# Optimization experiments

Hardware: AMD Instinct MI355X
Metric: run time of the kernel (lower is better)

## Reference

```python
import jax, jax.numpy as jnp
import numpy as np

D_MODEL = 1024
NUM_HEADS = 16
D_HEAD = D_MODEL // NUM_HEADS


def setup_inputs() -> dict:
    key = jax.random.key(0)
    ks = jax.random.split(key, 12)
    B, S, D = 2, 2048, D_MODEL
    s = 1.0 / np.sqrt(D)
    return {
        "Q": jax.random.normal(ks[0], (B, S, D), jnp.float32),
        "K": jax.random.normal(ks[1], (B, S, D), jnp.float32),
        "V": jax.random.normal(ks[2], (B, S, D), jnp.float32),
        "mask": jnp.ones((B, 1, 1, S), jnp.int32),
        "Wq": jax.random.normal(ks[3], (D, D), jnp.float32) * s,
        "bq": jnp.zeros((D,), jnp.float32),
        "Wk": jax.random.normal(ks[4], (D, D), jnp.float32) * s,
        "bk": jnp.zeros((D,), jnp.float32),
        "Wv": jax.random.normal(ks[5], (D, D), jnp.float32) * s,
        "bv": jnp.zeros((D,), jnp.float32),
        "Wo": jax.random.normal(ks[6], (D, D), jnp.float32) * s,
        "bo": jnp.zeros((D,), jnp.float32),
    }


def reference(Q, K, V, mask, Wq, bq, Wk, bk, Wv, bv, Wo, bo):
    B, Sq, D = Q.shape
    H, Dh = NUM_HEADS, D_HEAD
    # projections (torch Linear: x @ W.T + b), then split heads -> (B,H,S,Dh)
    q = (Q @ Wq.T + bq).reshape(B, Sq, H, Dh).transpose(0, 2, 1, 3)
    k = (K @ Wk.T + bk).reshape(B, -1, H, Dh).transpose(0, 2, 1, 3)
    v = (V @ Wv.T + bv).reshape(B, -1, H, Dh).transpose(0, 2, 1, 3)
    scores = jnp.einsum("bhqd,bhkd->bhqk", q, k) / jnp.sqrt(jnp.float32(Dh))
    scores = jnp.where(mask == 0, jnp.float32(-1e9), scores)
    attn = jax.nn.softmax(scores, axis=-1)
    out = jnp.einsum("bhqk,bhkd->bhqd", attn, v)  # (B,H,Sq,Dh)
    out = out.transpose(0, 2, 1, 3).reshape(B, Sq, D)
    out = out @ Wo.T + bo
    return out, attn
```

## Files before the change

### kernel.cpp

```cpp
#include <hip/hip_runtime.h>

#define BB 2
#define SS 2048
#define DD 1024
#define HH 16
#define DHH 64
#define NN (BB*SS)
#define NNDD ((size_t)NN * DD)
#define DDDD ((size_t)DD * DD)

typedef __attribute__((ext_vector_type(8))) __bf16 bf16x8;
typedef __attribute__((ext_vector_type(4))) float f32x4;
typedef union { unsigned int u[4]; bf16x8 v; } bfu8;

__device__ __forceinline__ unsigned short f2bf(float f) {
  unsigned int u = __float_as_uint(f);
  return (unsigned short)((u + 0x7FFFu + ((u >> 16) & 1u)) >> 16);
}
__device__ __forceinline__ float bf2f(unsigned short h) {
  return __uint_as_float(((unsigned int)h) << 16);
}

__device__ __forceinline__ void gl_lds16(const unsigned short* g, unsigned short* l) {
  __builtin_amdgcn_global_load_lds(
      (const __attribute__((address_space(1))) unsigned int*)g,
      (__attribute__((address_space(3))) unsigned int*)l, 16, 0, 0);
}

#define MFMA16(a, b, c) __builtin_amdgcn_mfma_f32_16x16x32_bf16((a), (b), (c), 0, 0, 0)

__global__ __launch_bounds__(256) void split3(
    const float* __restrict__ x0, const float* __restrict__ x1,
    const float* __restrict__ x2, unsigned short* __restrict__ outbase,
    size_t zstride, int n4) {
  const float* x = (blockIdx.z == 0) ? x0 : (blockIdx.z == 1 ? x1 : x2);
  unsigned short* hi = outbase + (size_t)blockIdx.z * zstride;
  unsigned short* lo = hi + (size_t)n4 * 4;
  int i = blockIdx.x * 256 + threadIdx.x;
  int stride = gridDim.x * 256;
  for (; i < n4; i += stride) {
    float4 v = ((const float4*)x)[i];
    float f[4] = {v.x, v.y, v.z, v.w};
    unsigned short hs[4], ls[4];
#pragma unroll
    for (int j = 0; j < 4; ++j) {
      hs[j] = f2bf(f[j]);
      ls[j] = f2bf(f[j] - bf2f(hs[j]));
    }
    ushort4 H, L;
    H.x = hs[0]; H.y = hs[1]; H.z = hs[2]; H.w = hs[3];
    L.x = ls[0]; L.y = ls[1]; L.z = ls[2]; L.w = ls[3];
    ((ushort4*)hi)[i] = H;
    ((ushort4*)lo)[i] = L;
  }
}

#define GBM 128
#define GBN 128
#define GBK 64

__global__ __launch_bounds__(256, 2) void gemm_bf16x3(
    const unsigned short* __restrict__ Abase, size_t aZstride,
    const unsigned short* __restrict__ Wbase, size_t wZstride,
    const float* __restrict__ b0, const float* __restrict__ b1,
    const float* __restrict__ b2,
    float* __restrict__ obase, size_t oZstride, int mode) {
  __shared__ __align__(16) unsigned short sAh[GBM * GBK];
  __shared__ __align__(16) unsigned short sAl[GBM * GBK];
  __shared__ __align__(16) unsigned short sBh[GBN * GBK];
  __shared__ __align__(16) unsigned short sBl[GBN * GBK];

  const int z = blockIdx.z;
  const unsigned short* Ah = Abase + (size_t)z * aZstride;
  const unsigned short* Al = Ah + NNDD;
  const unsigned short* Bh = Wbase + (size_t)z * wZstride;
  const unsigned short* Bl = Bh + DDDD;
  const float* bias = (z == 0) ? b0 : (z == 1 ? b1 : b2);
  float* out = obase + (size_t)z * oZstride;

  const int t  = threadIdx.x;
  const int l  = t & 63;
  const int w  = t >> 6;
  const int wr = w >> 1, wc = w & 1;
  const int m0 = blockIdx.y * GBM, n0 = blockIdx.x * GBN;

  const int lrow   = l >> 3;
  const int lchunk = (l & 7) ^ lrow;

  f32x4 acc[4][4] = {};

  const int NT = DD / GBK;
  for (int kt = 0; kt < NT; ++kt) {
    const int k0 = kt * GBK;
#pragma unroll
    for (int r = 0; r < 4; ++r) {
      int rowb = w * 32 + r * 8;
      size_t gA = (size_t)(m0 + rowb + lrow) * DD + k0 + lchunk * 8;
      size_t gB = (size_t)(n0 + rowb + lrow) * DD + k0 + lchunk * 8;
      int lo = rowb * 64;
      gl_lds16(Ah + gA, sAh + lo);
      gl_lds16(Al + gA, sAl + lo);
      gl_lds16(Bh + gB, sBh + lo);
      gl_lds16(Bl + gB, sBl + lo);
    }
    __syncthreads();

#pragma unroll
    for (int kk = 0; kk < 2; ++kk) {
      bf16x8 ah[4], al[4], bh[4], bl[4];
      const int ks = kk * 4 + (l >> 4);
      const int sw = (ks ^ (l & 7)) << 4;
#pragma unroll
      for (int f = 0; f < 4; ++f) {
        int ra = (wr * 64 + f * 16 + (l & 15)) * 128 + sw;
        int rb = (wc * 64 + f * 16 + (l & 15)) * 128 + sw;
        ah[f] = *(const bf16x8*)((const char*)sAh + ra);
        al[f] = *(const bf16x8*)((const char*)sAl + ra);
        bh[f] = *(const bf16x8*)((const char*)sBh + rb);
        bl[f] = *(const bf16x8*)((const char*)sBl + rb);
      }
#pragma unroll
      for (int fm = 0; fm < 4; ++fm)
#pragma unroll
        for (int fn = 0; fn < 4; ++fn) {
          acc[fm][fn] = MFMA16(ah[fm], bh[fn], acc[fm][fn]);
          acc[fm][fn] = MFMA16(ah[fm], bl[fn], acc[fm][fn]);
          acc[fm][fn] = MFMA16(al[fm], bh[fn], acc[fm][fn]);
        }
    }
    __syncthreads();
  }

#pragma unroll
  for (int fn = 0; fn < 4; ++fn) {
    int col = n0 + wc * 64 + fn * 16 + (l & 15);
    float bv = bias[col];
#pragma unroll
    for (int fm = 0; fm < 4; ++fm) {
      int rbase = m0 + wr * 64 + fm * 16 + (l >> 4) * 4;
#pragma unroll
      for (int r = 0; r < 4; ++r) {
        int row = rbase + r;
        float val = acc[fm][fn][r] + bv;
        if (mode == 0) {
          out[(size_t)row * DD + col] = val;
        } else {
          int bb = row >> 11, s2 = row & (SS - 1);
          int hh = col >> 6, dh = col & 63;
          size_t idx = (((size_t)(bb * HH + hh) * SS) + s2) * DHH + dh;
          unsigned short hp = f2bf(val);
          unsigned short lp = f2bf(val - bf2f(hp));
          if (z == 2) {
            ((unsigned int*)out)[idx] = ((unsigned int)hp << 16) | lp;
          } else {
            ((unsigned short*)out)[idx] = hp;
            (((unsigned short*)out) + NNDD)[idx] = lp;
          }
        }
      }
    }
  }
}

__global__ __launch_bounds__(256, 3) void attn_mfma(
    const unsigned short* __restrict__ qhi, const unsigned short* __restrict__ qlo,
    const unsigned short* __restrict__ khi, const unsigned short* __restrict__ klo,
    const unsigned int* __restrict__ vpk, const int* __restrict__ mask,
    float* __restrict__ attn_g,
    unsigned short* __restrict__ hiO, unsigned short* __restrict__ loO) {
  const int it = blockIdx.x;
  const int bh = blockIdx.y;
  const int b  = bh >> 4;
  const int h  = bh & 15;
  const int i0 = it * 64;

  __shared__ __align__(16) unsigned short sQ[2 * 4096];
  __shared__ __align__(16) unsigned int   uKP[64 * 68];
  __shared__ __align__(16) unsigned int   sVT[64 * 68];

  unsigned short* sQh = sQ;
  unsigned short* sQl = sQ + 4096;
  unsigned short* sKh = (unsigned short*)uKP;
  unsigned short* sKl = sKh + 4096;
  unsigned int*   sP  = uKP;

  const int t  = threadIdx.x;
  const int l  = t & 63;
  const int w  = t >> 6;
  const int lx = l & 15;
  const int ly = l >> 4;

  const int lrow   = l >> 3;
  const int lchunk = (l & 7) ^ lrow;

  {
    size_t gbase = ((size_t)bh * SS + i0) * DHH;
#pragma unroll
    for (int r = 0; r < 2; ++r) {
      int rowb = w * 16 + r * 8;
      size_t g = gbase + (size_t)(rowb + lrow) * DHH + lchunk * 8;
      gl_lds16(qhi + g, sQh + rowb * 64);
      gl_lds16(qlo + g, sQl + rowb * 64);
    }
  }

  float mreg[4], lreg[4];
#pragma unroll
  for (int r = 0; r < 4; ++r) { mreg[r] = -1e30f; lreg[r] = 0.f; }

  const float scale = 0.125f;

  for (int jt = 0; jt < 32; ++jt) {
    const int j0 = jt * 64;
    __syncthreads();
    {
      size_t gbase = ((size_t)bh * SS + j0) * DHH;
#pragma unroll
      for (int r = 0; r < 2; ++r) {
        int rowb = w * 16 + r * 8;
        size_t g = gbase + (size_t)(rowb + lrow) * DHH + lchunk * 8;
        gl_lds16(khi + g, sKh + rowb * 64);
        gl_lds16(klo + g, sKl + rowb * 64);
      }
    }
    __syncthreads();

    f32x4 accS[4] = {};
#pragma unroll
    for (int kk = 0; kk < 2; ++kk) {
      const int cs = ((kk * 4 + ly) ^ (l & 7)) * 8;
      bf16x8 ah = *(const bf16x8*)(sQh + (w * 16 + lx) * 64 + cs);
      bf16x8 al = *(const bf16x8*)(sQl + (w * 16 + lx) * 64 + cs);
#pragma unroll
      for (int fn = 0; fn < 4; ++fn) {
        bf16x8 kh = *(const bf16x8*)(sKh + (fn * 16 + lx) * 64 + cs);
        bf16x8 kl = *(const bf16x8*)(sKl + (fn * 16 + lx) * 64 + cs);
        accS[fn] = MFMA16(ah, kh, accS[fn]);
        accS[fn] = MFMA16(ah, kl, accS[fn]);
        accS[fn] = MFMA16(al, kh, accS[fn]);
      }
    }

    int mk[4];
#pragma unroll
    for (int fn = 0; fn < 4; ++fn) mk[fn] = mask[b * SS + j0 + fn * 16 + lx];
    float sc[4][4];
#pragma unroll
    for (int fn = 0; fn < 4; ++fn)
#pragma unroll
      for (int r = 0; r < 4; ++r) {
        float s = accS[fn][r] * scale;
        sc[fn][r] = (mk[fn] == 0) ? -1e9f : s;
      }
#pragma unroll
    for (int r = 0; r < 4; ++r) {
      float tm = fmaxf(fmaxf(sc[0][r], sc[1][r]), fmaxf(sc[2][r], sc[3][r]));
      tm = fmaxf(tm, __shfl_xor(tm, 1));
      tm = fmaxf(tm, __shfl_xor(tm, 2));
      tm = fmaxf(tm, __shfl_xor(tm, 4));
      tm = fmaxf(tm, __shfl_xor(tm, 8));
      float nm = fmaxf(mreg[r], tm);
      float ps = __expf(sc[0][r] - nm) + __expf(sc[1][r] - nm) +
                 __expf(sc[2][r] - nm) + __expf(sc[3][r] - nm);
      ps += __shfl_xor(ps, 1);
      ps += __shfl_xor(ps, 2);
      ps += __shfl_xor(ps, 4);
      ps += __shfl_xor(ps, 8);
      lreg[r] = lreg[r] * __expf(mreg[r] - nm) + ps;
      mreg[r] = nm;
    }
  }

  float invl[4];
#pragma unroll
  for (int r = 0; r < 4; ++r) invl[r] = 1.0f / lreg[r];

  f32x4 accO[4] = {};
  for (int jt = 0; jt < 32; ++jt) {
    const int j0 = jt * 64;
    __syncthreads();
    {
      size_t gbase = ((size_t)bh * SS + j0) * DHH;
#pragma unroll
      for (int r = 0; r < 2; ++r) {
        int rowb = w * 16 + r * 8;
        size_t g = gbase + (size_t)(rowb + lrow) * DHH + lchunk * 8;
        gl_lds16(khi + g, sKh + rowb * 64);
        gl_lds16(klo + g, sKl + rowb * 64);
      }
#pragma unroll
      for (int rr = 0; rr < 4; ++rr) {
        int j  = rr * 16 + (t >> 4);
        int c4 = t & 15;
        uint4 u = *(const uint4*)&vpk[((size_t)bh * SS + j0 + j) * DHH + c4 * 4];
        sVT[(c4 * 4 + 0) * 68 + j] = u.x;
        sVT[(c4 * 4 + 1) * 68 + j] = u.y;
        sVT[(c4 * 4 + 2) * 68 + j] = u.z;
        sVT[(c4 * 4 + 3) * 68 + j] = u.w;
      }
    }
    __syncthreads();

    f32x4 accS[4] = {};
#pragma unroll
    for (int kk = 0; kk < 2; ++kk) {
      const int cs = ((kk * 4 + ly) ^ (l & 7)) * 8;
      bf16x8 ah = *(const bf16x8*)(sQh + (w * 16 + lx) * 64 + cs);
      bf16x8 al = *(const bf16x8*)(sQl + (w * 16 + lx) * 64 + cs);
#pragma unroll
      for (int fn = 0; fn < 4; ++fn) {
        bf16x8 kh = *(const bf16x8*)(sKh + (fn * 16 + lx) * 64 + cs);
        bf16x8 kl = *(const bf16x8*)(sKl + (fn * 16 + lx) * 64 + cs);
        accS[fn] = MFMA16(ah, kh, accS[fn]);
        accS[fn] = MFMA16(ah, kl, accS[fn]);
        accS[fn] = MFMA16(al, kh, accS[fn]);
      }
    }

    int mk[4];
#pragma unroll
    for (int fn = 0; fn < 4; ++fn) mk[fn] = mask[b * SS + j0 + fn * 16 + lx];
    float p[4][4];
    float* arow = attn_g + ((size_t)bh * SS + i0 + w * 16) * SS + j0;
#pragma unroll
    for (int fn = 0; fn < 4; ++fn)
#pragma unroll
      for (int r = 0; r < 4; ++r) {
        float s = accS[fn][r] * scale;
        s = (mk[fn] == 0) ? -1e9f : s;
        float pv = __expf(s - mreg[r]) * invl[r];
        p[fn][r] = pv;
        arow[(size_t)(ly * 4 + r) * SS + fn * 16 + lx] = pv;
      }
    __syncthreads();

#pragma unroll
    for (int fn = 0; fn < 4; ++fn)
#pragma unroll
      for (int r = 0; r < 4; ++r) {
        unsigned short hp = f2bf(p[fn][r]);
        unsigned short lp = f2bf(p[fn][r] - bf2f(hp));
        sP[(w * 16 + ly * 4 + r) * 68 + fn * 16 + lx] =
            ((unsigned int)hp << 16) | lp;
      }

#pragma unroll
    for (int kk = 0; kk < 2; ++kk) {
      const int jb = kk * 32 + ly * 8;
      const unsigned int* pr = &sP[(w * 16 + lx) * 68 + jb];
      uint4 u0 = *(const uint4*)pr;
      uint4 u1 = *(const uint4*)(pr + 4);
      bfu8 pah, pal;
      pah.u[0] = (u0.x >> 16) | (u0.y & 0xFFFF0000u);
      pah.u[1] = (u0.z >> 16) | (u0.w & 0xFFFF0000u);
      pah.u[2] = (u1.x >> 16) | (u1.y & 0xFFFF0000u);
      pah.u[3] = (u1.z >> 16) | (u1.w & 0xFFFF0000u);
      pal.u[0] = (u0.x & 0xFFFFu) | (u0.y << 16);
      pal.u[1] = (u0.z & 0xFFFFu) | (u0.w << 16);
      pal.u[2] = (u1.x & 0xFFFFu) | (u1.y << 16);
      pal.u[3] = (u1.z & 0xFFFFu) | (u1.w << 16);
#pragma unroll
      for (int fn = 0; fn < 4; ++fn) {
        const unsigned int* vr = &sVT[(fn * 16 + lx) * 68 + jb];
        uint4 w0 = *(const uint4*)vr;
        uint4 w1 = *(const uint4*)(vr + 4);
        bfu8 vbh, vbl;
        vbh.u[0] = (w0.x >> 16) | (w0.y & 0xFFFF0000u);
        vbh.u[1] = (w0.z >> 16) | (w0.w & 0xFFFF0000u);
        vbh.u[2] = (w1.x >> 16) | (w1.y & 0xFFFF0000u);
        vbh.u[3] = (w1.z >> 16) | (w1.w & 0xFFFF0000u);
        vbl.u[0] = (w0.x & 0xFFFFu) | (w0.y << 16);
        vbl.u[1] = (w0.z & 0xFFFFu) | (w0.w << 16);
        vbl.u[2] = (w1.x & 0xFFFFu) | (w1.y << 16);
        vbl.u[3] = (w1.z & 0xFFFFu) | (w1.w << 16);
        accO[fn] = MFMA16(pah.v, vbh.v, accO[fn]);
        accO[fn] = MFMA16(pah.v, vbl.v, accO[fn]);
        accO[fn] = MFMA16(pal.v, vbh.v, accO[fn]);
      }
    }
  }

#pragma unroll
  for (int fn = 0; fn < 4; ++fn)
#pragma unroll
    for (int r = 0; r < 4; ++r) {
      float o = accO[fn][r];
      size_t idx = ((size_t)b * SS + i0 + w * 16 + ly * 4 + r) * DD +
                   h * DHH + fn * 16 + lx;
      unsigned short hp = f2bf(o);
      unsigned short lp = f2bf(o - bf2f(hp));
      hiO[idx] = hp;
      loO[idx] = lp;
    }
}

extern "C" void kernel_launch(void* const* d_in, const int* in_sizes, int n_in,
                              void* d_out, int out_size, void* d_ws, size_t ws_size,
                              hipStream_t stream) {
  const float* Q   = (const float*)d_in[0];
  const float* K   = (const float*)d_in[1];
  const float* V   = (const float*)d_in[2];
  const int*  mask = (const int*)d_in[3];
  const float* Wq  = (const float*)d_in[4];
  const float* bq  = (const float*)d_in[5];
  const float* Wk  = (const float*)d_in[6];
  const float* bk  = (const float*)d_in[7];
  const float* Wv  = (const float*)d_in[8];
  const float* bv  = (const float*)d_in[9];
  const float* Wo  = (const float*)d_in[10];
  const float* bo  = (const float*)d_in[11];

  float* out    = (float*)d_out;
  float* attn_g = out + NNDD;

  unsigned short* inPlanes = (unsigned short*)attn_g;
  unsigned short* wPlanes  = inPlanes + 6 * NNDD;

  float* ws = (float*)d_ws;
  unsigned short* qhi = (unsigned short*)ws;
  unsigned short* qlo = qhi + NNDD;
  unsigned short* khi = (unsigned short*)(ws + NNDD);
  unsigned short* klo = khi + NNDD;
  unsigned int*   vpk = (unsigned int*)(ws + 2 * NNDD);
  unsigned short* hiO = (unsigned short*)(ws + 3 * NNDD);
  unsigned short* loO = hiO + NNDD;
  unsigned short* woPlanes = (unsigned short*)ws;

  dim3 b256(256);

  hipLaunchKernelGGL(split3, dim3(1024, 1, 3), b256, 0, stream,
                     Wq, Wk, Wv, wPlanes, 2 * DDDD, (int)(DDDD / 4));
  hipLaunchKernelGGL(split3, dim3(2048, 1, 3), b256, 0, stream,
                     Q, K, V, inPlanes, 2 * NNDD, (int)(NNDD / 4));

  hipLaunchKernelGGL(gemm_bf16x3, dim3(DD / GBN, NN / GBM, 3), b256, 0, stream,
                     inPlanes, 2 * NNDD, wPlanes, 2 * DDDD,
                     bq, bk, bv, ws, NNDD, 1);

  hipLaunchKernelGGL(attn_mfma, dim3(32, 32), b256, 0, stream,
                     qhi, qlo, khi, klo, vpk, mask, attn_g, hiO, loO);

  hipLaunchKernelGGL(split3, dim3(1024, 1, 1), b256, 0, stream,
                     Wo, Wo, Wo, woPlanes, 0, (int)(DDDD / 4));
  hipLaunchKernelGGL(gemm_bf16x3, dim3(DD / GBN, NN / GBM, 1), b256, 0, stream,
                     hiO, 0, woPlanes, 0, bo, bo, bo, out, 0, 0);
}
```

Measured before the change: 1.062 ms.

## Double-buffer GEMM k-loop, pre-transpose V, swizzle P/V LDS, remap block order

```diff
diff --git a/kernel.cpp b/kernel.cpp
--- a/kernel.cpp
+++ b/kernel.cpp
@@ -11,7 +11,6 @@
 
 typedef __attribute__((ext_vector_type(8))) __bf16 bf16x8;
 typedef __attribute__((ext_vector_type(4))) float f32x4;
-typedef union { unsigned int u[4]; bf16x8 v; } bfu8;
 
 __device__ __forceinline__ unsigned short f2bf(float f) {
   unsigned int u = __float_as_uint(f);
@@ -55,9 +54,46 @@
   }
 }
 
+__global__ __launch_bounds__(256) void vtrans(
+    const unsigned short* __restrict__ src, unsigned short* __restrict__ dst) {
+  const unsigned short* s = src + (size_t)blockIdx.z * NNDD;
+  unsigned short* d = dst + (size_t)blockIdx.z * NNDD;
+  const int bh = blockIdx.y;
+  const int s0 = blockIdx.x * 64;
+  __shared__ unsigned short tile[64][68];
+  const int t = threadIdx.x;
+#pragma unroll
+  for (int r = 0; r < 2; ++r) {
+    int idx = t + 256 * r;
+    int srow = idx >> 3, c8 = idx & 7;
+    const unsigned short* sp = &s[((size_t)bh * SS + s0 + srow) * DHH + c8 * 8];
+    ushort4 u0 = *(const ushort4*)sp;
+    ushort4 u1 = *(const ushort4*)(sp + 4);
+    tile[c8*8+0][srow] = u0.x; tile[c8*8+1][srow] = u0.y;
+    tile[c8*8+2][srow] = u0.z; tile[c8*8+3][srow] = u0.w;
+    tile[c8*8+4][srow] = u1.x; tile[c8*8+5][srow] = u1.y;
+    tile[c8*8+6][srow] = u1.z; tile[c8*8+7][srow] = u1.w;
+  }
+  __syncthreads();
+#pragma unroll
+  for (int r = 0; r < 2; ++r) {
+    int idx = t + 256 * r;
+    int drow = idx >> 3, sc8 = idx & 7;
+    ushort4 o0, o1;
+    o0.x = tile[drow][sc8*8+0]; o0.y = tile[drow][sc8*8+1];
+    o0.z = tile[drow][sc8*8+2]; o0.w = tile[drow][sc8*8+3];
+    o1.x = tile[drow][sc8*8+4]; o1.y = tile[drow][sc8*8+5];
+    o1.z = tile[drow][sc8*8+6]; o1.w = tile[drow][sc8*8+7];
+    unsigned short* dp = &d[((size_t)bh * DHH + drow) * SS + s0 + sc8 * 8];
+    *(ushort4*)dp = o0;
+    *(ushort4*)(dp + 4) = o1;
+  }
+}
+
 #define GBM 128
 #define GBN 128
-#define GBK 64
+#define GBK 32
+#define GNT (DD / GBK)
 
 __global__ __launch_bounds__(256, 2) void gemm_bf16x3(
     const unsigned short* __restrict__ Abase, size_t aZstride,
@@ -65,12 +101,19 @@
     const float* __restrict__ b0, const float* __restrict__ b1,
     const float* __restrict__ b2,
     float* __restrict__ obase, size_t oZstride, int mode) {
-  __shared__ __align__(16) unsigned short sAh[GBM * GBK];
-  __shared__ __align__(16) unsigned short sAl[GBM * GBK];
-  __shared__ __align__(16) unsigned short sBh[GBN * GBK];
-  __shared__ __align__(16) unsigned short sBl[GBN * GBK];
-
-  const int z = blockIdx.z;
+  __shared__ __align__(16) unsigned short sAh[2 * 4096];
+  __shared__ __align__(16) unsigned short sAl[2 * 4096];
+  __shared__ __align__(16) unsigned short sBh[2 * 4096];
+  __shared__ __align__(16) unsigned short sBl[2 * 4096];
+
+  const int gx = gridDim.x, gy = gridDim.y;
+  int dlin = blockIdx.x + gx * (blockIdx.y + gy * blockIdx.z);
+  int nwg  = gx * gy * gridDim.z;
+  int o    = (dlin & 7) * (nwg >> 3) + (dlin >> 3);
+  int bx = o % gx; o /= gx;
+  int by = o % gy;
+  int z  = o / gy;
+
   const unsigned short* Ah = Abase + (size_t)z * aZstride;
   const unsigned short* Al = Ah + NNDD;
   const unsigned short* Bh = Wbase + (size_t)z * wZstride;
@@ -82,62 +125,72 @@
   const int l  = t & 63;
   const int w  = t >> 6;
   const int wr = w >> 1, wc = w & 1;
-  const int m0 = blockIdx.y * GBM, n0 = blockIdx.x * GBN;
-
-  const int lrow   = l >> 3;
-  const int lchunk = (l & 7) ^ lrow;
+  const int m0 = by * GBM, n0 = bx * GBN;
+
+  const int lrow4  = l >> 2;
+  const int gstage = (lrow4 ^ (lrow4 >> 2)) & 3;
+  const int lchunk = (l & 3) ^ gstage;
 
   f32x4 acc[4][4] = {};
 
-  const int NT = DD / GBK;
-  for (int kt = 0; kt < NT; ++kt) {
+  auto STAGE = [&](int kt, int buf) {
     const int k0 = kt * GBK;
-#pragma unroll
-    for (int r = 0; r < 4; ++r) {
-      int rowb = w * 32 + r * 8;
-      size_t gA = (size_t)(m0 + rowb + lrow) * DD + k0 + lchunk * 8;
-      size_t gB = (size_t)(n0 + rowb + lrow) * DD + k0 + lchunk * 8;
-      int lo = rowb * 64;
+    const int bo = buf * 4096;
+#pragma unroll
+    for (int r = 0; r < 2; ++r) {
+      int rowb = w * 32 + r * 16;
+      size_t gA = (size_t)(m0 + rowb + lrow4) * DD + k0 + lchunk * 8;
+      size_t gB = (size_t)(n0 + rowb + lrow4) * DD + k0 + lchunk * 8;
+      int lo = bo + rowb * 32;
       gl_lds16(Ah + gA, sAh + lo);
       gl_lds16(Al + gA, sAl + lo);
       gl_lds16(Bh + gB, sBh + lo);
       gl_lds16(Bl + gB, sBl + lo);
     }
-    __syncthreads();
-
-#pragma unroll
-    for (int kk = 0; kk < 2; ++kk) {
-      bf16x8 ah[4], al[4], bh[4], bl[4];
-      const int ks = kk * 4 + (l >> 4);
-      const int sw = (ks ^ (l & 7)) << 4;
-#pragma unroll
-      for (int f = 0; f < 4; ++f) {
-        int ra = (wr * 64 + f * 16 + (l & 15)) * 128 + sw;
-        int rb = (wc * 64 + f * 16 + (l & 15)) * 128 + sw;
-        ah[f] = *(const bf16x8*)((const char*)sAh + ra);
-        al[f] = *(const bf16x8*)((const char*)sAl + ra);
-        bh[f] = *(const bf16x8*)((const char*)sBh + rb);
-        bl[f] = *(const bf16x8*)((const char*)sBl + rb);
-      }
-#pragma unroll
-      for (int fm = 0; fm < 4; ++fm)
-#pragma unroll
-        for (int fn = 0; fn < 4; ++fn) {
-          acc[fm][fn] = MFMA16(ah[fm], bh[fn], acc[fm][fn]);
-          acc[fm][fn] = MFMA16(ah[fm], bl[fn], acc[fm][fn]);
-          acc[fm][fn] = MFMA16(al[fm], bh[fn], acc[fm][fn]);
-        }
-    }
+  };
+
+  const int lx = l & 15, ly = l >> 4;
+  const int gread = ((l & 3) ^ ((l >> 2) & 3));
+  const int cpos  = (ly ^ gread) << 3;
+
+  auto COMPUTE = [&](int buf) {
+    const int bo = buf * 4096;
+    bf16x8 ahf[4], alf[4], bhf[4], blf[4];
+#pragma unroll
+    for (int f = 0; f < 4; ++f) {
+      int ra = bo + (wr * 64 + f * 16 + lx) * 32 + cpos;
+      int rb = bo + (wc * 64 + f * 16 + lx) * 32 + cpos;
+      ahf[f] = *(const bf16x8*)(sAh + ra);
+      alf[f] = *(const bf16x8*)(sAl + ra);
+      bhf[f] = *(const bf16x8*)(sBh + rb);
+      blf[f] = *(const bf16x8*)(sBl + rb);
+    }
+#pragma unroll
+    for (int fm = 0; fm < 4; ++fm)
+#pragma unroll
+      for (int fn = 0; fn < 4; ++fn) {
+        acc[fm][fn] = MFMA16(ahf[fm], bhf[fn], acc[fm][fn]);
+        acc[fm][fn] = MFMA16(ahf[fm], blf[fn], acc[fm][fn]);
+        acc[fm][fn] = MFMA16(alf[fm], bhf[fn], acc[fm][fn]);
+      }
+  };
+
+  STAGE(0, 0);
+  __syncthreads();
+  for (int kt = 0; kt < GNT; ++kt) {
+    int cur = kt & 1;
+    if (kt + 1 < GNT) STAGE(kt + 1, cur ^ 1);
+    COMPUTE(cur);
     __syncthreads();
   }
 
 #pragma unroll
   for (int fn = 0; fn < 4; ++fn) {
-    int col = n0 + wc * 64 + fn * 16 + (l & 15);
+    int col = n0 + wc * 64 + fn * 16 + lx;
     float bv = bias[col];
 #pragma unroll
     for (int fm = 0; fm < 4; ++fm) {
-      int rbase = m0 + wr * 64 + fm * 16 + (l >> 4) * 4;
+      int rbase = m0 + wr * 64 + fm * 16 + ly * 4;
 #pragma unroll
       for (int r = 0; r < 4; ++r) {
         int row = rbase + r;
@@ -149,13 +202,8 @@
           int hh = col >> 6, dh = col & 63;
           size_t idx = (((size_t)(bb * HH + hh) * SS) + s2) * DHH + dh;
           unsigned short hp = f2bf(val);
-          unsigned short lp = f2bf(val - bf2f(hp));
-          if (z == 2) {
-            ((unsigned int*)out)[idx] = ((unsigned int)hp << 16) | lp;
-          } else {
-            ((unsigned short*)out)[idx] = hp;
-            (((unsigned short*)out) + NNDD)[idx] = lp;
-          }
+          ((unsigned short*)out)[idx] = hp;
+          (((unsigned short*)out) + NNDD)[idx] = f2bf(val - bf2f(hp));
         }
       }
     }
@@ -165,31 +213,28 @@
 __global__ __launch_bounds__(256, 3) void attn_mfma(
     const unsigned short* __restrict__ qhi, const unsigned short* __restrict__ qlo,
     const unsigned short* __restrict__ khi, const unsigned short* __restrict__ klo,
-    const unsigned int* __restrict__ vpk, const int* __restrict__ mask,
-    float* __restrict__ attn_g,
+    const unsigned short* __restrict__ vthi, const unsigned short* __restrict__ vtlo,
+    const int* __restrict__ mask, float* __restrict__ attn_g,
     unsigned short* __restrict__ hiO, unsigned short* __restrict__ loO) {
-  const int it = blockIdx.x;
-  const int bh = blockIdx.y;
+  int dlin = blockIdx.x + 32 * blockIdx.y;
+  int o    = (dlin & 7) * 128 + (dlin >> 3);
+  const int it = o & 31;
+  const int bh = o >> 5;
   const int b  = bh >> 4;
   const int h  = bh & 15;
   const int i0 = it * 64;
 
-  __shared__ __align__(16) unsigned short sQ[2 * 4096];
-  __shared__ __align__(16) unsigned int   uKP[64 * 68];
-  __shared__ __align__(16) unsigned int   sVT[64 * 68];
-
-  unsigned short* sQh = sQ;
-  unsigned short* sQl = sQ + 4096;
-  unsigned short* sKh = (unsigned short*)uKP;
-  unsigned short* sKl = sKh + 4096;
-  unsigned int*   sP  = uKP;
+  __shared__ __align__(16) unsigned short sQh[4096], sQl[4096];
+  __shared__ __align__(16) unsigned short sKP[8192];
+  __shared__ __align__(16) unsigned short sVh[4096], sVl[4096];
+  unsigned short* sKh = sKP;
+  unsigned short* sKl = sKP + 4096;
 
   const int t  = threadIdx.x;
   const int l  = t & 63;
   const int w  = t >> 6;
   const int lx = l & 15;
   const int ly = l >> 4;
-
   const int lrow   = l >> 3;
   const int lchunk = (l & 7) ^ lrow;
 
@@ -284,19 +329,12 @@
 #pragma unroll
       for (int r = 0; r < 2; ++r) {
         int rowb = w * 16 + r * 8;
-        size_t g = gbase + (size_t)(rowb + lrow) * DHH + lchunk * 8;
+        size_t g  = gbase + (size_t)(rowb + lrow) * DHH + lchunk * 8;
+        size_t gv = ((size_t)bh * DHH + rowb + lrow) * SS + j0 + lchunk * 8;
         gl_lds16(khi + g, sKh + rowb * 64);
         gl_lds16(klo + g, sKl + rowb * 64);
-      }
-#pragma unroll
-      for (int rr = 0; rr < 4; ++rr) {
-        int j  = rr * 16 + (t >> 4);
-        int c4 = t & 15;
-        uint4 u = *(const uint4*)&vpk[((size_t)bh * SS + j0 + j) * DHH + c4 * 4];
-        sVT[(c4 * 4 + 0) * 68 + j] = u.x;
-        sVT[(c4 * 4 + 1) * 68 + j] = u.y;
-        sVT[(c4 * 4 + 2) * 68 + j] = u.z;
-        sVT[(c4 * 4 + 3) * 68 + j] = u.w;
+        gl_lds16(vthi + gv, sVh + rowb * 64);
+        gl_lds16(vtlo + gv, sVl + rowb * 64);
       }
     }
     __syncthreads();
@@ -338,44 +376,26 @@
     for (int fn = 0; fn < 4; ++fn)
 #pragma unroll
       for (int r = 0; r < 4; ++r) {
+        int prow = w * 16 + ly * 4 + r;
+        int pcol = fn * 16 + lx;
+        int pos  = (((pcol >> 3) ^ (prow & 7)) << 3) + (pcol & 7);
         unsigned short hp = f2bf(p[fn][r]);
-        unsigned short lp = f2bf(p[fn][r] - bf2f(hp));
-        sP[(w * 16 + ly * 4 + r) * 68 + fn * 16 + lx] =
-            ((unsigned int)hp << 16) | lp;
+        sKP[prow * 64 + pos] = hp;
+        sKP[4096 + prow * 64 + pos] = f2bf(p[fn][r] - bf2f(hp));
       }
 
 #pragma unroll
     for (int kk = 0; kk < 2; ++kk) {
-      const int jb = kk * 32 + ly * 8;
-      const unsigned int* pr = &sP[(w * 16 + lx) * 68 + jb];
-      uint4 u0 = *(const uint4*)pr;
-      uint4 u1 = *(const uint4*)(pr + 4);
-      bfu8 pah, pal;
-      pah.u[0] = (u0.x >> 16) | (u0.y & 0xFFFF0000u);
-      pah.u[1] = (u0.z >> 16) | (u0.w & 0xFFFF0000u);
-      pah.u[2] = (u1.x >> 16) | (u1.y & 0xFFFF0000u);
-      pah.u[3] = (u1.z >> 16) | (u1.w & 0xFFFF0000u);
-      pal.u[0] = (u0.x & 0xFFFFu) | (u0.y << 16);
-      pal.u[1] = (u0.z & 0xFFFFu) | (u0.w << 16);
-      pal.u[2] = (u1.x & 0xFFFFu) | (u1.y << 16);
-      pal.u[3] = (u1.z & 0xFFFFu) | (u1.w << 16);
+      const int cs = ((kk * 4 + ly) ^ (l & 7)) * 8;
+      bf16x8 pah = *(const bf16x8*)(sKP + (w * 16 + lx) * 64 + cs);
+      bf16x8 pal = *(const bf16x8*)(sKP + 4096 + (w * 16 + lx) * 64 + cs);
 #pragma unroll
       for (int fn = 0; fn < 4; ++fn) {
-        const unsigned int* vr = &sVT[(fn * 16 + lx) * 68 + jb];
-        uint4 w0 = *(const uint4*)vr;
-        uint4 w1 = *(const uint4*)(vr + 4);
-        bfu8 vbh, vbl;
-        vbh.u[0] = (w0.x >> 16) | (w0.y & 0xFFFF0000u);
-        vbh.u[1] = (w0.z >> 16) | (w0.w & 0xFFFF0000u);
-        vbh.u[2] = (w1.x >> 16) | (w1.y & 0xFFFF0000u);
-        vbh.u[3] = (w1.z >> 16) | (w1.w & 0xFFFF0000u);
-        vbl.u[0] = (w0.x & 0xFFFFu) | (w0.y << 16);
-        vbl.u[1] = (w0.z & 0xFFFFu) | (w0.w << 16);
-        vbl.u[2] = (w1.x & 0xFFFFu) | (w1.y << 16);
-        vbl.u[3] = (w1.z & 0xFFFFu) | (w1.w << 16);
-        accO[fn] = MFMA16(pah.v, vbh.v, accO[fn]);
-        accO[fn] = MFMA16(pah.v, vbl.v, accO[fn]);
-        accO[fn] = MFMA16(pal.v, vbh.v, accO[fn]);
+        bf16x8 vbh = *(const bf16x8*)(sVh + (fn * 16 + lx) * 64 + cs);
+        bf16x8 vbl = *(const bf16x8*)(sVl + (fn * 16 + lx) * 64 + cs);
+        accO[fn] = MFMA16(pah, vbh, accO[fn]);
+        accO[fn] = MFMA16(pah, vbl, accO[fn]);
+        accO[fn] = MFMA16(pal, vbh, accO[fn]);
       }
     }
   }
@@ -384,13 +404,12 @@
   for (int fn = 0; fn < 4; ++fn)
 #pragma unroll
     for (int r = 0; r < 4; ++r) {
-      float o = accO[fn][r];
+      float ov = accO[fn][r];
       size_t idx = ((size_t)b * SS + i0 + w * 16 + ly * 4 + r) * DD +
                    h * DHH + fn * 16 + lx;
-      unsigned short hp = f2bf(o);
-      unsigned short lp = f2bf(o - bf2f(hp));
+      unsigned short hp = f2bf(ov);
       hiO[idx] = hp;
-      loO[idx] = lp;
+      loO[idx] = f2bf(ov - bf2f(hp));
     }
 }
 
@@ -417,14 +436,10 @@
   unsigned short* wPlanes  = inPlanes + 6 * NNDD;
 
   float* ws = (float*)d_ws;
-  unsigned short* qhi = (unsigned short*)ws;
-  unsigned short* qlo = qhi + NNDD;
-  unsigned short* khi = (unsigned short*)(ws + NNDD);
-  unsigned short* klo = khi + NNDD;
-  unsigned int*   vpk = (unsigned int*)(ws + 2 * NNDD);
-  unsigned short* hiO = (unsigned short*)(ws + 3 * NNDD);
-  unsigned short* loO = hiO + NNDD;
-  unsigned short* woPlanes = (unsigned short*)ws;
+  unsigned short* qPl  = (unsigned short*)ws;
+  unsigned short* kPl  = (unsigned short*)(ws + NNDD);
+  unsigned short* vPl  = (unsigned short*)(ws + 2 * NNDD);
+  unsigned short* vtPl = (unsigned short*)(ws + 3 * NNDD);
 
   dim3 b256(256);
 
@@ -437,11 +452,15 @@
                      inPlanes, 2 * NNDD, wPlanes, 2 * DDDD,
                      bq, bk, bv, ws, NNDD, 1);
 
+  hipLaunchKernelGGL(vtrans, dim3(SS / 64, BB * HH, 2), b256, 0, stream,
+                     vPl, vtPl);
+
   hipLaunchKernelGGL(attn_mfma, dim3(32, 32), b256, 0, stream,
-                     qhi, qlo, khi, klo, vpk, mask, attn_g, hiO, loO);
+                     qPl, qPl + NNDD, kPl, kPl + NNDD, vtPl, vtPl + NNDD,
+                     mask, attn_g, vPl, vPl + NNDD);
 
   hipLaunchKernelGGL(split3, dim3(1024, 1, 1), b256, 0, stream,
-                     Wo, Wo, Wo, woPlanes, 0, (int)(DDDD / 4));
+                     Wo, Wo, Wo, qPl, 0, (int)(DDDD / 4));
   hipLaunchKernelGGL(gemm_bf16x3, dim3(DD / GBN, NN / GBM, 1), b256, 0, stream,
-                     hiO, 0, woPlanes, 0, bo, bo, bo, out, 0, 0);
-}
+                     vPl, 0, qPl, 0, bo, bo, bo, out, 0, 0);
+}
```

Measured after the change: 1.037 ms. 1.02x faster.
